# Kernel optimization log

Hardware: AMD Instinct MI355X
Metric: run time of the kernel (lower is better)

## Reference

```python
import jax, jax.numpy as jnp
import numpy as np

NUM_EMBED = 54012  # hardcoded self.num_nodes in GraphNet
IN_FEATS = 256
HID = 32           # hardcoded gcn1 output width
OUT_FEATS = 256
N_NODES = 65536
N_EDGES = 1048576
BATCH = 4096


def setup_inputs() -> dict:
    key = jax.random.key(0)
    ks = jax.random.split(key, 12)
    # graph structure (int args)
    idx = jax.random.randint(ks[0], (N_NODES,), 0, NUM_EMBED)
    src = jax.random.randint(ks[1], (N_EDGES,), 0, N_NODES)
    dst = jax.random.randint(ks[2], (N_EDGES,), 0, N_NODES)
    gene1_idx = jax.random.randint(ks[3], (BATCH,), 0, N_NODES)
    gene2_idx = jax.random.randint(ks[4], (BATCH,), 0, N_NODES)
    # learned parameters (xavier-ish scaling)
    embed = jax.random.normal(ks[5], (NUM_EMBED, IN_FEATS), jnp.float32) * (2.0 / (NUM_EMBED + IN_FEATS)) ** 0.5
    W1 = jax.random.normal(ks[6], (IN_FEATS, HID), jnp.float32) * (2.0 / (IN_FEATS + HID)) ** 0.5
    b1 = jnp.zeros((HID,), jnp.float32)
    W2 = jax.random.normal(ks[7], (HID, OUT_FEATS), jnp.float32) * (2.0 / (HID + OUT_FEATS)) ** 0.5
    b2 = jnp.zeros((OUT_FEATS,), jnp.float32)
    Wfc = jax.random.normal(ks[8], (2 * OUT_FEATS, OUT_FEATS), jnp.float32) * (2.0 / (3 * OUT_FEATS)) ** 0.5
    bfc = jnp.zeros((OUT_FEATS,), jnp.float32)
    return dict(idx=idx, src=src, dst=dst, gene1_idx=gene1_idx, gene2_idx=gene2_idx,
                embed=embed, W1=W1, b1=b1, W2=W2, b2=b2, Wfc=Wfc, bfc=bfc)


def _spmm_sum(feat, src, dst, n):
    # DGL copy_u + sum: out[v] = sum over edges (u->v) of feat[u]
    return jax.ops.segment_sum(feat[src], dst, num_segments=n)


def reference(idx, src, dst, gene1_idx, gene2_idx, embed, W1, b1, W2, b2, Wfc, bfc):
    n = idx.shape[0]
    feat = embed[idx]                              # [N, in_feats]
    # GCN layer 1: aggregate -> linear -> relu
    h = jax.nn.relu(_spmm_sum(feat, src, dst, n) @ W1 + b1)   # [N, 32]
    # GCN layer 2: aggregate -> linear (no activation)
    h2 = _spmm_sum(h, src, dst, n) @ W2 + b2                  # [N, out_feats]
    # per-graph SL gene pair gather + concat + linear + relu
    pair = jnp.concatenate([h2[gene1_idx], h2[gene2_idx]], axis=1)  # [B, 2*out_feats]
    return jax.nn.relu(pair @ Wfc + bfc)                      # [B, out_feats]
```

## Files before the change

### kernel.cpp

```cpp
#include <hip/hip_runtime.h>

#define IN_FEATS 256
#define HID 32
#define NUM_EMBED 54012
#define N_NODES 65536
#define N_EDGES 1048576
#define BATCH 4096

#define NR 256
#define NB 512
#define EPB (N_EDGES / NB)
#define PBCAP 32
#define HCAP 24
#define OVF_CAP 65536
#define GEMMB 844
#define NTILE 3376
#define W1P 272

typedef unsigned short u16t;
typedef unsigned int u32t;
typedef __attribute__((ext_vector_type(8))) short bf16x8;
typedef __attribute__((ext_vector_type(4))) float f32x4;

__device__ __forceinline__ float bf2f(u16t u) {
    return __uint_as_float(((u32t)u) << 16);
}
__device__ __forceinline__ u16t f2bf(float f) {
    u32t x = __float_as_uint(f);
    return (u16t)((x + 0x7FFFu + ((x >> 16) & 1u)) >> 16);
}
__device__ __forceinline__ u32t cvt_pk(float lo, float hi) {
    u32t r;
    asm("v_cvt_pk_bf16_f32 %0, %1, %2" : "=v"(r) : "v"(lo), "v"(hi));
    return r;
}

__device__ __forceinline__ float half_sum_bf(const int4* cell, int m,
                                             const u16t* __restrict__ feat1, int c) {
    int4 c0 = cell[0];
    u32t w[4] = {(u32t)c0.x, (u32t)c0.y, (u32t)c0.z, (u32t)c0.w};
    float va[8];
#pragma unroll
    for (int k = 0; k < 4; ++k) {
        va[2 * k + 0] = bf2f(feat1[((size_t)(w[k] & 0xFFFFu) << 5) + c]);
        va[2 * k + 1] = bf2f(feat1[((size_t)(w[k] >> 16) << 5) + c]);
    }
    float acc = 0.f;
#pragma unroll
    for (int j = 0; j < 8; ++j) acc += (m > j) ? va[j] : 0.f;
    if (m > 8) {
        int4 c1 = cell[1];
        u32t x[4] = {(u32t)c1.x, (u32t)c1.y, (u32t)c1.z, (u32t)c1.w};
        float vb[8];
#pragma unroll
        for (int k = 0; k < 4; ++k) {
            vb[2 * k + 0] = bf2f(feat1[((size_t)(x[k] & 0xFFFFu) << 5) + c]);
            vb[2 * k + 1] = bf2f(feat1[((size_t)(x[k] >> 16) << 5) + c]);
        }
#pragma unroll
        for (int j = 0; j < 8; ++j) acc += (m > 8 + j) ? vb[j] : 0.f;
        if (m > 16) {
            int4 c2 = cell[2];
            u32t y[4] = {(u32t)c2.x, (u32t)c2.y, (u32t)c2.z, (u32t)c2.w};
            float vc[8];
#pragma unroll
            for (int k = 0; k < 4; ++k) {
                vc[2 * k + 0] = bf2f(feat1[((size_t)(y[k] & 0xFFFFu) << 5) + c]);
                vc[2 * k + 1] = bf2f(feat1[((size_t)(y[k] >> 16) << 5) + c]);
            }
#pragma unroll
            for (int j = 0; j < 8; ++j) acc += (m > 16 + j) ? vc[j] : 0.f;
        }
    }
    return acc;
}

__device__ __forceinline__ float half_sum_f32(const int4* cell, int m,
                                              const float* __restrict__ agg1, int c) {
    int4 c0 = cell[0];
    u32t w[4] = {(u32t)c0.x, (u32t)c0.y, (u32t)c0.z, (u32t)c0.w};
    float va[8];
#pragma unroll
    for (int k = 0; k < 4; ++k) {
        va[2 * k + 0] = agg1[((size_t)(w[k] & 0xFFFFu) << 5) + c];
        va[2 * k + 1] = agg1[((size_t)(w[k] >> 16) << 5) + c];
    }
    float acc = 0.f;
#pragma unroll
    for (int j = 0; j < 8; ++j) acc += (m > j) ? va[j] : 0.f;
    if (m > 8) {
        int4 c1 = cell[1];
        u32t x[4] = {(u32t)c1.x, (u32t)c1.y, (u32t)c1.z, (u32t)c1.w};
        float vb[8];
#pragma unroll
        for (int k = 0; k < 4; ++k) {
            vb[2 * k + 0] = agg1[((size_t)(x[k] & 0xFFFFu) << 5) + c];
            vb[2 * k + 1] = agg1[((size_t)(x[k] >> 16) << 5) + c];
        }
#pragma unroll
        for (int j = 0; j < 8; ++j) acc += (m > 8 + j) ? vb[j] : 0.f;
        if (m > 16) {
            int4 c2 = cell[2];
            u32t y[4] = {(u32t)c2.x, (u32t)c2.y, (u32t)c2.z, (u32t)c2.w};
            float vc[8];
#pragma unroll
            for (int k = 0; k < 4; ++k) {
                vc[2 * k + 0] = agg1[((size_t)(y[k] & 0xFFFFu) << 5) + c];
                vc[2 * k + 1] = agg1[((size_t)(y[k] >> 16) << 5) + c];
            }
#pragma unroll
            for (int j = 0; j < 8; ++j) acc += (m > 16 + j) ? vc[j] : 0.f;
        }
    }
    return acc;
}

__global__ void k_phaseA(const float* __restrict__ embed, const float* __restrict__ W1,
                         u16t* __restrict__ tmpb,
                         const int* __restrict__ src, const int* __restrict__ dst,
                         u32t* __restrict__ subseg, u16t* __restrict__ hcnt,
                         int* __restrict__ ovf_cnt, int* __restrict__ ovf,
                         const float* __restrict__ W2, const float* __restrict__ b2,
                         const float* __restrict__ Wfc, const float* __restrict__ bfc,
                         float* __restrict__ M1, float* __restrict__ M2,
                         float* __restrict__ bias) {
    __shared__ __align__(16) char smem[32 * W1P * 2];
    int b = blockIdx.x;
    int t = threadIdx.x;

    if (b < NB) {
        int bb = b;
        u32t* hist = (u32t*)smem;
        u32t* cur  = hist + 256;
        u32t* epak = cur + 256;
        unsigned char* erng = (unsigned char*)(epak + EPB);
        hist[t] = 0;
        cur[t] = 0;
        __syncthreads();
        int base = bb * EPB;
#pragma unroll
        for (int k = 0; k < EPB / 256; ++k) {
            int i = k * 256 + t;
            int s = __builtin_nontemporal_load(&src[base + i]);
            int d = __builtin_nontemporal_load(&dst[base + i]);
            int r = d >> 8;
            epak[i] = (u32t)s | ((u32t)(d & 255) << 16);
            erng[i] = (unsigned char)r;
            atomicAdd(&hist[r], 1u);
        }
        __syncthreads();
        hcnt[t * NB + bb] = (u16t)min(hist[t], (u32t)PBCAP);
#pragma unroll
        for (int k = 0; k < EPB / 256; ++k) {
            int i = k * 256 + t;
            u32t w = epak[i];
            int r = erng[i];
            u32t p = atomicAdd(&cur[r], 1u);
            if (p < PBCAP) {
                subseg[((size_t)((u32t)r * NB + bb)) * PBCAP + p] = w;
            } else {
                int o = atomicAdd(ovf_cnt, 1);
                u32t dfull = ((u32t)r << 8) | (w >> 16);
                if (o < OVF_CAP) ovf[o] = (int)((w & 0xFFFFu) | (dfull << 16));
            }
        }
    } else if (b < NB + GEMMB) {
        u16t* w1t = (u16t*)smem;
        for (int i = t; i < IN_FEATS * HID; i += 256) {
            int k = i >> 5, c = i & 31;
            w1t[c * W1P + k] = f2bf(W1[i]);
        }
        __syncthreads();

        int lane = t & 63;
        int wv = t >> 6;
        int tile = (b - NB) * 4 + wv;
        if (tile >= NTILE) return;
        int r0 = tile * 16;

        int arow = min(r0 + (lane & 15), NUM_EMBED - 1);
        int kq = (lane >> 4) * 8;
        const float* Erow = embed + (size_t)arow * IN_FEATS + kq;

        int c = lane & 15;
        bf16x8 bf0[8], bf1[8];
        {
            const u16t* bp0 = w1t + (size_t)c * W1P + kq;
            const u16t* bp1 = w1t + (size_t)(c + 16) * W1P + kq;
#pragma unroll
            for (int kk = 0; kk < 8; ++kk) {
                bf0[kk] = *(const bf16x8*)(bp0 + kk * 32);
                bf1[kk] = *(const bf16x8*)(bp1 + kk * 32);
            }
        }

        f32x4 acc0 = {0.f, 0.f, 0.f, 0.f};
        f32x4 acc1 = {0.f, 0.f, 0.f, 0.f};
#pragma unroll
        for (int kk = 0; kk < 8; ++kk) {
            float4 p = *(const float4*)(Erow + kk * 32);
            float4 q = *(const float4*)(Erow + kk * 32 + 4);
            union { bf16x8 v; u32t u[4]; } a;
            a.u[0] = cvt_pk(p.x, p.y);
            a.u[1] = cvt_pk(p.z, p.w);
            a.u[2] = cvt_pk(q.x, q.y);
            a.u[3] = cvt_pk(q.z, q.w);
            acc0 = __builtin_amdgcn_mfma_f32_16x16x32_bf16(a.v, bf0[kk], acc0, 0, 0, 0);
            acc1 = __builtin_amdgcn_mfma_f32_16x16x32_bf16(a.v, bf1[kk], acc1, 0, 0, 0);
        }

        int rbase = r0 + (lane >> 4) * 4;
#pragma unroll
        for (int j = 0; j < 4; ++j) {
            int rr = rbase + j;
            if (rr < NUM_EMBED) {
                tmpb[(size_t)rr * HID + c]      = f2bf(acc0[j]);
                tmpb[(size_t)rr * HID + 16 + c] = f2bf(acc1[j]);
            }
        }
    } else {
        int r = b - NB - GEMMB;
        int c = t;
        if (r < 32) {
            float p0 = 0.f, p1 = 0.f, p2 = 0.f, p3 = 0.f;
#pragma unroll
            for (int j = 0; j < 256; j += 4) {
                p0 += W2[r * 256 + j + 0] * Wfc[(j + 0) * 256 + c];
                p1 += W2[r * 256 + j + 1] * Wfc[(j + 1) * 256 + c];
                p2 += W2[r * 256 + j + 2] * Wfc[(j + 2) * 256 + c];
                p3 += W2[r * 256 + j + 3] * Wfc[(j + 3) * 256 + c];
            }
            M1[r * 256 + c] = (p0 + p1) + (p2 + p3);
        } else if (r < 64) {
            int k = r - 32;
            float p0 = 0.f, p1 = 0.f, p2 = 0.f, p3 = 0.f;
#pragma unroll
            for (int j = 0; j < 256; j += 4) {
                p0 += W2[k * 256 + j + 0] * Wfc[(256 + j + 0) * 256 + c];
                p1 += W2[k * 256 + j + 1] * Wfc[(256 + j + 1) * 256 + c];
                p2 += W2[k * 256 + j + 2] * Wfc[(256 + j + 2) * 256 + c];
                p3 += W2[k * 256 + j + 3] * Wfc[(256 + j + 3) * 256 + c];
            }
            M2[k * 256 + c] = (p0 + p1) + (p2 + p3);
        } else {
            if (t == 0) *ovf_cnt = 0;
            float p0 = 0.f, p1 = 0.f;
#pragma unroll
            for (int j = 0; j < 256; j += 2) {
                p0 += b2[j + 0] * (Wfc[(j + 0) * 256 + c] + Wfc[(256 + j + 0) * 256 + c]);
                p1 += b2[j + 1] * (Wfc[(j + 1) * 256 + c] + Wfc[(256 + j + 1) * 256 + c]);
            }
            bias[c] = bfc[c] + p0 + p1;
        }
    }
}

__global__ void k_phaseB(const u32t* __restrict__ subseg, const u16t* __restrict__ hcnt,
                         u32t* __restrict__ cntAB, u16t* __restrict__ bins2,
                         int* __restrict__ ovf_cnt, int* __restrict__ ovf,
                         const u32t* __restrict__ tmpu, const int* __restrict__ idx,
                         u32t* __restrict__ feat1u) {
    __shared__ u16t cells[NR * HCAP];
    __shared__ u32t cl[NR];
    __shared__ u16t hc[NB / 2];
    int b = blockIdx.x;
    int t = threadIdx.x;
    if (b < 2 * NR) {
        int r = b >> 1, h = b & 1;
        for (int i = t; i < NR * HCAP / 2; i += 256) ((u32t*)cells)[i] = 0;
        cl[t] = 0;
        if (t < 128)
            ((u32t*)hc)[t] = ((const u32t*)(hcnt + (size_t)r * NB + h * 256))[t];
        __syncthreads();

        const u32t* segr = subseg + ((size_t)r * NB + h * 256) * PBCAP;
        for (int base_lin = 0; base_lin < 256 * PBCAP; base_lin += 2048) {
            u32t wbuf[8];
            int vld[8];
#pragma unroll
            for (int u = 0; u < 8; ++u) {
                int lin = base_lin + u * 256 + t;
                int bb = lin >> 5;
                int slot = lin & (PBCAP - 1);
                vld[u] = (slot < (int)hc[bb]);
                wbuf[u] = __builtin_nontemporal_load(&segr[lin]);
            }
#pragma unroll
            for (int u = 0; u < 8; ++u) {
                if (vld[u]) {
                    u32t w = wbuf[u];
                    int dl = (int)(w >> 16) & 255;
                    u32t p = atomicAdd(&cl[dl], 1u);
                    if (p < HCAP) {
                        cells[dl * HCAP + p] = (u16t)(w & 0xFFFFu);
                    } else {
                        int o = atomicAdd(ovf_cnt, 1);
                        u32t dfull = ((u32t)r << 8) | (u32t)dl;
                        if (o < OVF_CAP) ovf[o] = (int)((w & 0xFFFFu) | (dfull << 16));
                    }
                }
            }
        }
        __syncthreads();
        u32t* dst32 = (u32t*)(bins2) + ((size_t)h * N_NODES + ((size_t)r << 8)) * (HCAP / 2);
        for (int i = t; i < NR * HCAP / 2; i += 256)
            dst32[i] = ((const u32t*)cells)[i];
        ((u16t*)cntAB)[(((size_t)r << 8) + t) * 2 + h] = (u16t)min(cl[t], 65535u);
    } else {
        int i = (b - 2 * NR) * 256 + t;
        int n = i >> 4, j = i & 15;
        feat1u[((size_t)n << 4) + j] = tmpu[((size_t)idx[n] << 4) + j];
    }
}

__global__ void k_spmm1(const u16t* __restrict__ feat1,
                        const u32t* __restrict__ cntAB, const u16t* __restrict__ bins2,
                        const int* __restrict__ ovf_cnt, const int* __restrict__ ovf,
                        const float* __restrict__ b1, float* __restrict__ agg1) {
    int t = blockIdx.x * 256 + threadIdx.x;
    int v = t >> 5, c = t & 31;
    u32t cw = cntAB[v];
    int mA = min((int)(cw & 0xFFFFu), HCAP);
    int mB = min((int)(cw >> 16), HCAP);
    const int4* cellA = (const int4*)(bins2 + (size_t)v * HCAP);
    const int4* cellB = (const int4*)(bins2 + ((size_t)N_NODES + v) * HCAP);
    float acc = half_sum_bf(cellA, mA, feat1, c) + half_sum_bf(cellB, mB, feat1, c);

    int total = min(*ovf_cnt, OVF_CAP);
    for (int i = 0; i < total; ++i) {
        u32t e = (u32t)ovf[i];
        if ((e >> 16) == (u32t)v)
            acc += bf2f(feat1[((size_t)(e & 0xFFFFu) << 5) + c]);
    }
    agg1[t] = fmaxf(acc + b1[c], 0.f);
}

__global__ void k_tail(const float* __restrict__ agg1,
                       const u32t* __restrict__ cntAB, const u16t* __restrict__ bins2,
                       const int* __restrict__ ovf_cnt, const int* __restrict__ ovf,
                       const int* __restrict__ g1, const int* __restrict__ g2,
                       const float* __restrict__ M1, const float* __restrict__ M2,
                       const float* __restrict__ bias,
                       float* __restrict__ out) {
    __shared__ float a1s[8][HID];
    __shared__ float a2s[8][HID];
    int i0 = blockIdx.x * 8;
    int tid = threadIdx.x;
    int sg = tid >> 5, c = tid & 31;

    for (int side = 0; side < 2; ++side) {
        int slot = i0 + sg;
        int v = side ? g2[slot] : g1[slot];
        u32t cw = cntAB[v];
        int mA = min((int)(cw & 0xFFFFu), HCAP);
        int mB = min((int)(cw >> 16), HCAP);
        const int4* cellA = (const int4*)(bins2 + (size_t)v * HCAP);
        const int4* cellB = (const int4*)(bins2 + ((size_t)N_NODES + v) * HCAP);
        float acc = half_sum_f32(cellA, mA, agg1, c) + half_sum_f32(cellB, mB, agg1, c);

        int total = min(*ovf_cnt, OVF_CAP);
        for (int i = 0; i < total; ++i) {
            u32t e = (u32t)ovf[i];
            if ((e >> 16) == (u32t)v)
                acc += agg1[((size_t)(e & 0xFFFFu) << 5) + c];
        }
        if (side) a2s[sg][c] = acc;
        else      a1s[sg][c] = acc;
    }
    __syncthreads();

    int cc = tid;
    float acc[8];
#pragma unroll
    for (int q = 0; q < 8; ++q) acc[q] = bias[cc];
#pragma unroll
    for (int k = 0; k < HID; ++k) {
        float m1 = M1[k * 256 + cc];
        float m2 = M2[k * 256 + cc];
#pragma unroll
        for (int q = 0; q < 8; ++q)
            acc[q] += a1s[q][k] * m1 + a2s[q][k] * m2;
    }
#pragma unroll
    for (int q = 0; q < 8; ++q)
        out[(size_t)(i0 + q) * 256 + cc] = fmaxf(acc[q], 0.f);
}

extern "C" void kernel_launch(void* const* d_in, const int* in_sizes, int n_in,
                              void* d_out, int out_size, void* d_ws, size_t ws_size,
                              hipStream_t stream) {
    const int*   idx   = (const int*)d_in[0];
    const int*   src   = (const int*)d_in[1];
    const int*   dst   = (const int*)d_in[2];
    const int*   g1    = (const int*)d_in[3];
    const int*   g2    = (const int*)d_in[4];
    const float* embed = (const float*)d_in[5];
    const float* W1    = (const float*)d_in[6];
    const float* b1    = (const float*)d_in[7];
    const float* W2    = (const float*)d_in[8];
    const float* b2    = (const float*)d_in[9];
    const float* Wfc   = (const float*)d_in[10];
    const float* bfc   = (const float*)d_in[11];
    float* out = (float*)d_out;

    char* ws = (char*)d_ws;
    u16t*  tmpb     = (u16t*)ws;   ws += (size_t)NUM_EMBED * HID * 2 + 64;
    u16t*  feat1    = (u16t*)ws;   ws += (size_t)N_NODES * HID * 2;
    float* agg1     = (float*)ws;  ws += (size_t)N_NODES * HID * 4;
    float* M1       = (float*)ws;  ws += 32 * 256 * 4;
    float* M2       = (float*)ws;  ws += 32 * 256 * 4;
    float* bias     = (float*)ws;  ws += 256 * 4;
    u32t*  subseg   = (u32t*)ws;   ws += (size_t)NR * NB * PBCAP * 4;
    u16t*  hcnt     = (u16t*)ws;   ws += (size_t)NR * NB * 2;
    u32t*  cntAB    = (u32t*)ws;   ws += (size_t)N_NODES * 4;
    u16t*  bins2    = (u16t*)ws;   ws += (size_t)2 * N_NODES * HCAP * 2;
    int*   ovf_cnt  = (int*)ws;    ws += 64;
    int*   ovf      = (int*)ws;    ws += (size_t)OVF_CAP * 4;

    k_phaseA<<<NB + GEMMB + 65, 256, 0, stream>>>(embed, W1, tmpb,
                                                  src, dst, subseg, hcnt, ovf_cnt, ovf,
                                                  W2, b2, Wfc, bfc, M1, M2, bias);

    k_phaseB<<<2 * NR + (N_NODES * 16) / 256, 256, 0, stream>>>(subseg, hcnt,
                                                                cntAB, bins2,
                                                                ovf_cnt, ovf,
                                                                (const u32t*)tmpb, idx,
                                                                (u32t*)feat1);

    k_spmm1<<<(N_NODES * 32) / 256, 256, 0, stream>>>(feat1, cntAB, bins2,
                                                      ovf_cnt, ovf, b1, agg1);

    k_tail<<<BATCH / 8, 256, 0, stream>>>(agg1, cntAB, bins2, ovf_cnt, ovf,
                                          g1, g2, M1, M2, bias, out);
}
```

Before: 71.63 us.

## Fuse embedding gather into W1 GEMM, computing per-node features directly

The W1 projection now runs per node, reading embedding rows through idx, so the GEMM writes feat1 directly. This removes the intermediate per-embedding tmpb buffer and the separate gather blocks in the second kernel, which becomes a pure edge-packing kernel. The cost is more GEMM tiles (65536 rows instead of 54012) and scattered embedding row reads. The W1 staging into shared memory also switches to float4 loads.

```diff
diff --git a/kernel.cpp b/kernel.cpp
--- a/kernel.cpp
+++ b/kernel.cpp
@@ -13,8 +13,8 @@
 #define PBCAP 32
 #define HCAP 24
 #define OVF_CAP 65536
-#define GEMMB 844
-#define NTILE 3376
+#define GEMMB 1024
+#define NTILEN 4096
 #define W1P 272
 
 typedef unsigned short u16t;
@@ -116,7 +116,7 @@
 }
 
 __global__ void k_phaseA(const float* __restrict__ embed, const float* __restrict__ W1,
-                         u16t* __restrict__ tmpb,
+                         const int* __restrict__ idx, u16t* __restrict__ feat1,
                          const int* __restrict__ src, const int* __restrict__ dst,
                          u32t* __restrict__ subseg, u16t* __restrict__ hcnt,
                          int* __restrict__ ovf_cnt, int* __restrict__ ovf,
@@ -166,19 +166,24 @@
         }
     } else if (b < NB + GEMMB) {
         u16t* w1t = (u16t*)smem;
-        for (int i = t; i < IN_FEATS * HID; i += 256) {
+        for (int i4 = t; i4 < IN_FEATS * HID / 4; i4 += 256) {
+            float4 v = ((const float4*)W1)[i4];
+            int i = i4 * 4;
             int k = i >> 5, c = i & 31;
-            w1t[c * W1P + k] = f2bf(W1[i]);
+            w1t[(c + 0) * W1P + k] = f2bf(v.x);
+            w1t[(c + 1) * W1P + k] = f2bf(v.y);
+            w1t[(c + 2) * W1P + k] = f2bf(v.z);
+            w1t[(c + 3) * W1P + k] = f2bf(v.w);
         }
         __syncthreads();
 
         int lane = t & 63;
         int wv = t >> 6;
         int tile = (b - NB) * 4 + wv;
-        if (tile >= NTILE) return;
-        int r0 = tile * 16;
-
-        int arow = min(r0 + (lane & 15), NUM_EMBED - 1);
+        int n0 = tile * 16;
+
+        int node = n0 + (lane & 15);
+        int arow = idx[node];
         int kq = (lane >> 4) * 8;
         const float* Erow = embed + (size_t)arow * IN_FEATS + kq;
 
@@ -209,14 +214,12 @@
             acc1 = __builtin_amdgcn_mfma_f32_16x16x32_bf16(a.v, bf1[kk], acc1, 0, 0, 0);
         }
 
-        int rbase = r0 + (lane >> 4) * 4;
+        int rbase = n0 + (lane >> 4) * 4;
 #pragma unroll
         for (int j = 0; j < 4; ++j) {
             int rr = rbase + j;
-            if (rr < NUM_EMBED) {
-                tmpb[(size_t)rr * HID + c]      = f2bf(acc0[j]);
-                tmpb[(size_t)rr * HID + 16 + c] = f2bf(acc1[j]);
-            }
+            feat1[(size_t)rr * HID + c]      = f2bf(acc0[j]);
+            feat1[(size_t)rr * HID + 16 + c] = f2bf(acc1[j]);
         }
     } else {
         int r = b - NB - GEMMB;
@@ -255,62 +258,54 @@
     }
 }
 
-__global__ void k_phaseB(const u32t* __restrict__ subseg, const u16t* __restrict__ hcnt,
-                         u32t* __restrict__ cntAB, u16t* __restrict__ bins2,
-                         int* __restrict__ ovf_cnt, int* __restrict__ ovf,
-                         const u32t* __restrict__ tmpu, const int* __restrict__ idx,
-                         u32t* __restrict__ feat1u) {
+__global__ void k_pack(const u32t* __restrict__ subseg, const u16t* __restrict__ hcnt,
+                       u32t* __restrict__ cntAB, u16t* __restrict__ bins2,
+                       int* __restrict__ ovf_cnt, int* __restrict__ ovf) {
     __shared__ u16t cells[NR * HCAP];
     __shared__ u32t cl[NR];
     __shared__ u16t hc[NB / 2];
     int b = blockIdx.x;
     int t = threadIdx.x;
-    if (b < 2 * NR) {
-        int r = b >> 1, h = b & 1;
-        for (int i = t; i < NR * HCAP / 2; i += 256) ((u32t*)cells)[i] = 0;
-        cl[t] = 0;
-        if (t < 128)
-            ((u32t*)hc)[t] = ((const u32t*)(hcnt + (size_t)r * NB + h * 256))[t];
-        __syncthreads();
-
-        const u32t* segr = subseg + ((size_t)r * NB + h * 256) * PBCAP;
-        for (int base_lin = 0; base_lin < 256 * PBCAP; base_lin += 2048) {
-            u32t wbuf[8];
-            int vld[8];
-#pragma unroll
-            for (int u = 0; u < 8; ++u) {
-                int lin = base_lin + u * 256 + t;
-                int bb = lin >> 5;
-                int slot = lin & (PBCAP - 1);
-                vld[u] = (slot < (int)hc[bb]);
-                wbuf[u] = __builtin_nontemporal_load(&segr[lin]);
-            }
-#pragma unroll
-            for (int u = 0; u < 8; ++u) {
-                if (vld[u]) {
-                    u32t w = wbuf[u];
-                    int dl = (int)(w >> 16) & 255;
-                    u32t p = atomicAdd(&cl[dl], 1u);
-                    if (p < HCAP) {
-                        cells[dl * HCAP + p] = (u16t)(w & 0xFFFFu);
-                    } else {
-                        int o = atomicAdd(ovf_cnt, 1);
-                        u32t dfull = ((u32t)r << 8) | (u32t)dl;
-                        if (o < OVF_CAP) ovf[o] = (int)((w & 0xFFFFu) | (dfull << 16));
-                    }
+    int r = b >> 1, h = b & 1;
+    for (int i = t; i < NR * HCAP / 2; i += 256) ((u32t*)cells)[i] = 0;
+    cl[t] = 0;
+    if (t < 128)
+        ((u32t*)hc)[t] = ((const u32t*)(hcnt + (size_t)r * NB + h * 256))[t];
+    __syncthreads();
+
+    const u32t* segr = subseg + ((size_t)r * NB + h * 256) * PBCAP;
+    for (int base_lin = 0; base_lin < 256 * PBCAP; base_lin += 2048) {
+        u32t wbuf[8];
+        int vld[8];
+#pragma unroll
+        for (int u = 0; u < 8; ++u) {
+            int lin = base_lin + u * 256 + t;
+            int bb = lin >> 5;
+            int slot = lin & (PBCAP - 1);
+            vld[u] = (slot < (int)hc[bb]);
+            wbuf[u] = __builtin_nontemporal_load(&segr[lin]);
+        }
+#pragma unroll
+        for (int u = 0; u < 8; ++u) {
+            if (vld[u]) {
+                u32t w = wbuf[u];
+                int dl = (int)(w >> 16) & 255;
+                u32t p = atomicAdd(&cl[dl], 1u);
+                if (p < HCAP) {
+                    cells[dl * HCAP + p] = (u16t)(w & 0xFFFFu);
+                } else {
+                    int o = atomicAdd(ovf_cnt, 1);
+                    u32t dfull = ((u32t)r << 8) | (u32t)dl;
+                    if (o < OVF_CAP) ovf[o] = (int)((w & 0xFFFFu) | (dfull << 16));
                 }
             }
         }
-        __syncthreads();
-        u32t* dst32 = (u32t*)(bins2) + ((size_t)h * N_NODES + ((size_t)r << 8)) * (HCAP / 2);
-        for (int i = t; i < NR * HCAP / 2; i += 256)
-            dst32[i] = ((const u32t*)cells)[i];
-        ((u16t*)cntAB)[(((size_t)r << 8) + t) * 2 + h] = (u16t)min(cl[t], 65535u);
-    } else {
-        int i = (b - 2 * NR) * 256 + t;
-        int n = i >> 4, j = i & 15;
-        feat1u[((size_t)n << 4) + j] = tmpu[((size_t)idx[n] << 4) + j];
-    }
+    }
+    __syncthreads();
+    u32t* dst32 = (u32t*)(bins2) + ((size_t)h * N_NODES + ((size_t)r << 8)) * (HCAP / 2);
+    for (int i = t; i < NR * HCAP / 2; i += 256)
+        dst32[i] = ((const u32t*)cells)[i];
+    ((u16t*)cntAB)[(((size_t)r << 8) + t) * 2 + h] = (u16t)min(cl[t], 65535u);
 }
 
 __global__ void k_spmm1(const u16t* __restrict__ feat1,
@@ -404,7 +399,6 @@
     float* out = (float*)d_out;
 
     char* ws = (char*)d_ws;
-    u16t*  tmpb     = (u16t*)ws;   ws += (size_t)NUM_EMBED * HID * 2 + 64;
     u16t*  feat1    = (u16t*)ws;   ws += (size_t)N_NODES * HID * 2;
     float* agg1     = (float*)ws;  ws += (size_t)N_NODES * HID * 4;
     float* M1       = (float*)ws;  ws += 32 * 256 * 4;
@@ -417,15 +411,11 @@
     int*   ovf_cnt  = (int*)ws;    ws += 64;
     int*   ovf      = (int*)ws;    ws += (size_t)OVF_CAP * 4;
 
-    k_phaseA<<<NB + GEMMB + 65, 256, 0, stream>>>(embed, W1, tmpb,
+    k_phaseA<<<NB + GEMMB + 65, 256, 0, stream>>>(embed, W1, idx, feat1,
                                                   src, dst, subseg, hcnt, ovf_cnt, ovf,
                                                   W2, b2, Wfc, bfc, M1, M2, bias);
 
-    k_phaseB<<<2 * NR + (N_NODES * 16) / 256, 256, 0, stream>>>(subseg, hcnt,
-                                                                cntAB, bins2,
-                                                                ovf_cnt, ovf,
-                                                                (const u32t*)tmpb, idx,
-                                                                (u32t*)feat1);
+    k_pack<<<2 * NR, 256, 0, stream>>>(subseg, hcnt, cntAB, bins2, ovf_cnt, ovf);
 
     k_spmm1<<<(N_NODES * 32) / 256, 256, 0, stream>>>(feat1, cntAB, bins2,
                                                       ovf_cnt, ovf, b1, agg1);
```

Measured after the change: 75.40 us. 1.05x slower.
